# Optimization experiments

Measured on AMD Instinct MI355X. Metric: run time of the kernel, lower is better.

## Reference

```python
import jax, jax.numpy as jnp
import numpy as np

N_EXPERTS = 8
TOPK = 2
W_IMPORTANCE = 0.01
W_LOAD = 0.01
LAMBDA_Z = 0.001
W_PENALTY = 0.01
PENALTY_TEMP = 1.66


def setup_inputs() -> dict:
    key = jax.random.key(0)
    ks = jax.random.split(key, 8)
    B, S, D, H, E = 8, 4096, 512, 2048, N_EXPERTS
    T = B * S
    return {
        "x": jax.random.normal(ks[0], (B, S, D), dtype=jnp.float32),
        "gate_w": jax.random.normal(ks[1], (E, D), dtype=jnp.float32) * 0.02,
        "noise_w": jax.random.normal(ks[2], (E, D), dtype=jnp.float32) * 0.02,
        "bias": jnp.zeros((E,), dtype=jnp.float32),
        "c_fc_w": jax.random.normal(ks[3], (E, H, D), dtype=jnp.float32) * 0.02,
        "c_fc_b": jnp.zeros((E, H), dtype=jnp.float32),
        "c_proj_w": jax.random.normal(ks[4], (E, D, H), dtype=jnp.float32) * 0.02,
        "c_proj_b": jnp.zeros((E, D), dtype=jnp.float32),
        "noise": jax.random.normal(ks[5], (T, E), dtype=jnp.float32),
    }


def reference(x, gate_w, noise_w, bias, c_fc_w, c_fc_b, c_proj_w, c_proj_b, noise):
    E, K = N_EXPERTS, TOPK
    D = x.shape[-1]
    xs = x.reshape(-1, D)                      # [T, D]
    T = xs.shape[0]

    gate_logits = xs @ gate_w.T                # [T, E]

    # penalty (pre-noise logits)
    p = jax.nn.softmax(gate_logits / PENALTY_TEMP, axis=-1)
    penalty_a = jnp.mean(p * (1.0 - p))
    pm = p.mean(axis=0)
    penalty_b = 1.0 / E - jnp.mean(pm * (1.0 - pm))
    penalty = (penalty_a + penalty_b) * W_PENALTY

    # z-loss (pre-noise logits)
    lse = jax.scipy.special.logsumexp(gate_logits, axis=-1)
    z_loss = LAMBDA_Z * jnp.mean(lse ** 2)

    # noisy gating + bias
    noise_std = jax.nn.softplus(xs @ noise_w.T)
    gate_logits = gate_logits + noise * noise_std + bias

    weights_vals, selected = jax.lax.top_k(gate_logits, K)   # [T, K]
    weights = jax.nn.softmax(weights_vals.astype(jnp.float32), axis=1).astype(x.dtype)

    # importance loss: scatter-add weights per expert
    importance = jax.ops.segment_sum(weights.reshape(-1), selected.reshape(-1),
                                     num_segments=E)
    cv2 = jnp.var(importance) / jnp.mean(importance) ** 2
    importance_loss = W_IMPORTANCE * cv2

    # load loss: top-1 counts vs mean router probs (post-noise)
    router_probs = jax.nn.softmax(gate_logits.astype(jnp.float32), axis=-1).astype(x.dtype)
    top1 = selected[:, 0]
    fi = jax.ops.segment_sum(jnp.ones((T,), dtype=jnp.float32), top1,
                             num_segments=E) / T
    load_loss = W_LOAD * E * jnp.sum(fi * router_probs.mean(axis=0))

    aux = penalty + z_loss + importance_loss + load_loss

    # combine weights per (token, expert): [T, E]
    comb = jnp.zeros((T, E), dtype=x.dtype).at[jnp.arange(T)[:, None], selected].add(weights)

    results = jnp.zeros_like(xs)
    for e in range(E):  # fixed small expert count
        h = jax.nn.gelu(xs @ c_fc_w[e].T + c_fc_b[e], approximate=True)
        o = h @ c_proj_w[e].T + c_proj_b[e]
        results = results + comb[:, e:e + 1] * o

    return results.reshape(x.shape), aux
```

## Files before the change

kernel.cpp:

```cpp
#include <hip/hip_runtime.h>
#include <hip/hip_bf16.h>
#include <stdint.h>

#define TTOK 32768
#define DDIM 512
#define HDIM 2048
#define NEXP 8
#define GBLK 1024

typedef __attribute__((ext_vector_type(4))) float f32x4;
typedef __attribute__((ext_vector_type(8))) short bf16x8;

#define GLOAD16(gp, lp)                                                      \
  __builtin_amdgcn_global_load_lds(                                          \
      (const __attribute__((address_space(1))) unsigned int*)(gp),           \
      (__attribute__((address_space(3))) unsigned int*)(lp), 16, 0, 0)

__device__ __forceinline__ ushort f2bf(float f) {
  union { float f; uint32_t u; } cv; cv.f = f;
  uint32_t u = cv.u;
  u = u + 0x7fffu + ((u >> 16) & 1u);
  return (ushort)(u >> 16);
}

__device__ __forceinline__ float bf2f(ushort u) {
  union { uint32_t u; float f; } cv; cv.u = ((uint32_t)u) << 16;
  return cv.f;
}

__device__ __forceinline__ float gelu_fast(float v) {
  float y = 1.5957691216057308f * (v + 0.044715f * v * v * v);
  return v / (1.0f + __expf(-y));
}

__global__ __launch_bounds__(256) void cvtw_kernel(const float* __restrict__ src,
                                                   ushort* __restrict__ dst, int n4) {
  int i = blockIdx.x * blockDim.x + threadIdx.x;
  if (i >= n4) return;
  float4 v = reinterpret_cast<const float4*>(src)[i];
  ushort4 o;
  o.x = f2bf(v.x); o.y = f2bf(v.y); o.z = f2bf(v.z); o.w = f2bf(v.w);
  reinterpret_cast<ushort4*>(dst)[i] = o;
}

__global__ __launch_bounds__(256, 2) void gating_kernel(
    const float* __restrict__ x, const float* __restrict__ gw,
    const float* __restrict__ nw, const float* __restrict__ bias,
    const float* __restrict__ noise, ushort* __restrict__ xbf,
    int* __restrict__ cnt, int* __restrict__ idxl,
    int2* __restrict__ slots, float2* __restrict__ tokw,
    float* __restrict__ part) {
  const int tid = threadIdx.x;
  const int lane = tid & 63;
  const int wave = tid >> 6;

  float wg[NEXP][8], wn[NEXP][8];
#pragma unroll
  for (int e = 0; e < NEXP; ++e) {
    const float4* pg = reinterpret_cast<const float4*>(gw + e * DDIM + lane * 8);
    float4 g0 = pg[0], g1 = pg[1];
    wg[e][0] = g0.x; wg[e][1] = g0.y; wg[e][2] = g0.z; wg[e][3] = g0.w;
    wg[e][4] = g1.x; wg[e][5] = g1.y; wg[e][6] = g1.z; wg[e][7] = g1.w;
    const float4* pq = reinterpret_cast<const float4*>(nw + e * DDIM + lane * 8);
    float4 n0 = pq[0], n1 = pq[1];
    wn[e][0] = n0.x; wn[e][1] = n0.y; wn[e][2] = n0.z; wn[e][3] = n0.w;
    wn[e][4] = n1.x; wn[e][5] = n1.y; wn[e][6] = n1.z; wn[e][7] = n1.w;
  }
  float bia[NEXP];
#pragma unroll
  for (int e = 0; e < NEXP; ++e) bia[e] = bias[e];

  float pa_s = 0.f, z_s = 0.f;
  float pm_s[NEXP], imp_s[NEXP], rp_s[NEXP], c1_s[NEXP];
#pragma unroll
  for (int e = 0; e < NEXP; ++e) { pm_s[e] = 0.f; imp_s[e] = 0.f; rp_s[e] = 0.f; c1_s[e] = 0.f; }

  __shared__ int s_i1[32], s_i2[32];
  __shared__ float s_w1[32], s_w2[32];
  __shared__ int lcnt[NEXP], lpos1[32], lpos2[32], gbase[NEXP];

  const int t00 = blockIdx.x * 32 + wave * 8;
  for (int it = 0; it < 8; it += 2) {
    float xv[2][8], nz[2][8];
#pragma unroll
    for (int u = 0; u < 2; ++u) {
      const int t = t00 + it + u;
      const float4* np = reinterpret_cast<const float4*>(noise + (size_t)t * NEXP);
      float4 nz0 = np[0], nz1 = np[1];
      nz[u][0] = nz0.x; nz[u][1] = nz0.y; nz[u][2] = nz0.z; nz[u][3] = nz0.w;
      nz[u][4] = nz1.x; nz[u][5] = nz1.y; nz[u][6] = nz1.z; nz[u][7] = nz1.w;
      const float4* xp = reinterpret_cast<const float4*>(x + (size_t)t * DDIM + lane * 8);
      float4 x0 = xp[0], x1 = xp[1];
      xv[u][0] = x0.x; xv[u][1] = x0.y; xv[u][2] = x0.z; xv[u][3] = x0.w;
      xv[u][4] = x1.x; xv[u][5] = x1.y; xv[u][6] = x1.z; xv[u][7] = x1.w;
      ushort u8[8];
#pragma unroll
      for (int j = 0; j < 8; ++j) u8[j] = f2bf(xv[u][j]);
      uint4 pack;
      pack.x = (uint32_t)u8[0] | ((uint32_t)u8[1] << 16);
      pack.y = (uint32_t)u8[2] | ((uint32_t)u8[3] << 16);
      pack.z = (uint32_t)u8[4] | ((uint32_t)u8[5] << 16);
      pack.w = (uint32_t)u8[6] | ((uint32_t)u8[7] << 16);
      *reinterpret_cast<uint4*>(xbf + (size_t)t * DDIM + lane * 8) = pack;
    }

    float pg[2][NEXP], pn[2][NEXP];
#pragma unroll
    for (int u = 0; u < 2; ++u)
#pragma unroll
      for (int e = 0; e < NEXP; ++e) { pg[u][e] = 0.f; pn[u][e] = 0.f; }
#pragma unroll
    for (int e = 0; e < NEXP; ++e)
#pragma unroll
      for (int j = 0; j < 8; ++j) {
#pragma unroll
        for (int u = 0; u < 2; ++u) {
          pg[u][e] = fmaf(xv[u][j], wg[e][j], pg[u][e]);
          pn[u][e] = fmaf(xv[u][j], wn[e][j], pn[u][e]);
        }
      }
#pragma unroll
    for (int m = 1; m < 64; m <<= 1) {
#pragma unroll
      for (int u = 0; u < 2; ++u)
#pragma unroll
        for (int e = 0; e < NEXP; ++e) {
          pg[u][e] += __shfl_xor(pg[u][e], m);
          pn[u][e] += __shfl_xor(pn[u][e], m);
        }
    }

#pragma unroll
    for (int u = 0; u < 2; ++u) {
      const int t = t00 + it + u;
      float sv[NEXP];
#pragma unroll
      for (int e = 0; e < NEXP; ++e) sv[e] = pg[u][e] * (1.0f / 1.66f);
      float mx = sv[0];
#pragma unroll
      for (int e = 1; e < NEXP; ++e) mx = fmaxf(mx, sv[e]);
      float ssum = 0.f, pvals[NEXP];
#pragma unroll
      for (int e = 0; e < NEXP; ++e) { pvals[e] = __expf(sv[e] - mx); ssum += pvals[e]; }
      float sinv = 1.f / ssum;
#pragma unroll
      for (int e = 0; e < NEXP; ++e) {
        float pe = pvals[e] * sinv;
        pa_s += pe * (1.f - pe);
        pm_s[e] += pe;
      }
      float mg = pg[u][0];
#pragma unroll
      for (int e = 1; e < NEXP; ++e) mg = fmaxf(mg, pg[u][e]);
      float es2 = 0.f;
#pragma unroll
      for (int e = 0; e < NEXP; ++e) es2 += __expf(pg[u][e] - mg);
      float lse = mg + __logf(es2);
      z_s += lse * lse;
      float g2[NEXP];
#pragma unroll
      for (int e = 0; e < NEXP; ++e) {
        float s = pn[u][e];
        float sp = fmaxf(s, 0.f) + __logf(1.f + __expf(-fabsf(s)));
        g2[e] = pg[u][e] + nz[u][e] * sp + bia[e];
      }
      float v1 = g2[0]; int i1 = 0;
#pragma unroll
      for (int e = 1; e < NEXP; ++e) if (g2[e] > v1) { v1 = g2[e]; i1 = e; }
      float v2 = -3.4e38f; int i2 = 0;
#pragma unroll
      for (int e = 0; e < NEXP; ++e) if (e != i1 && g2[e] > v2) { v2 = g2[e]; i2 = e; }
      float dd = __expf(v2 - v1);
      float w1 = 1.f / (1.f + dd);
      float w2 = dd / (1.f + dd);
      float mr = g2[0];
#pragma unroll
      for (int e = 1; e < NEXP; ++e) mr = fmaxf(mr, g2[e]);
      float rs = 0.f, er[NEXP];
#pragma unroll
      for (int e = 0; e < NEXP; ++e) { er[e] = __expf(g2[e] - mr); rs += er[e]; }
      float rinv = 1.f / rs;
#pragma unroll
      for (int e = 0; e < NEXP; ++e) rp_s[e] += er[e] * rinv;
#pragma unroll
      for (int e = 0; e < NEXP; ++e) {
        imp_s[e] += (e == i1 ? w1 : 0.f) + (e == i2 ? w2 : 0.f);
        c1_s[e] += (e == i1) ? 1.f : 0.f;
      }
      if (lane == 0) {
        int k = wave * 8 + it + u;
        s_i1[k] = i1; s_i2[k] = i2; s_w1[k] = w1; s_w2[k] = w2;
      }
    }
  }

  __shared__ float red[4][34];
  if (lane == 0) {
    red[wave][0] = pa_s; red[wave][1] = z_s;
#pragma unroll
    for (int e = 0; e < NEXP; ++e) {
      red[wave][2 + e] = pm_s[e];
      red[wave][10 + e] = imp_s[e];
      red[wave][18 + e] = rp_s[e];
      red[wave][26 + e] = c1_s[e];
    }
  }
  if (tid < NEXP) lcnt[tid] = 0;
  __syncthreads();
  if (tid < 34) {
    float s = red[0][tid] + red[1][tid] + red[2][tid] + red[3][tid];
    part[(size_t)tid * GBLK + blockIdx.x] = s;
  }
  if (tid < 32) {
    lpos1[tid] = atomicAdd(&lcnt[s_i1[tid]], 1);
    lpos2[tid] = atomicAdd(&lcnt[s_i2[tid]], 1);
  }
  __syncthreads();
  if (tid < NEXP) gbase[tid] = atomicAdd(&cnt[tid], lcnt[tid]);
  __syncthreads();
  if (tid < 32) {
    int t = blockIdx.x * 32 + tid;
    int e1 = s_i1[tid], p1 = gbase[e1] + lpos1[tid];
    int e2 = s_i2[tid], p2 = gbase[e2] + lpos2[tid];
    idxl[e1 * TTOK + p1] = t;
    idxl[e2 * TTOK + p2] = t;
    slots[t] = make_int2((e1 << 16) | p1, (e2 << 16) | p2);
    tokw[t] = make_float2(s_w1[tid], s_w2[tid]);
  }
}

__global__ __launch_bounds__(256) void finalize_kernel(
    const float* __restrict__ part, const int* __restrict__ cnt,
    int* __restrict__ offs, int* __restrict__ idxl,
    float* __restrict__ aux_out) {
  __shared__ float sums[34];
  __shared__ float red[4][34];
  __shared__ int roundc[NEXP], base[NEXP];
  const int tid = threadIdx.x;
  const int lane = tid & 63, wave = tid >> 6;

  float loc[34];
#pragma unroll
  for (int s = 0; s < 34; ++s) loc[s] = 0.f;
  for (int b = tid; b < GBLK; b += 256) {
#pragma unroll
    for (int s = 0; s < 34; ++s) loc[s] += part[(size_t)s * GBLK + b];
  }
#pragma unroll
  for (int m = 1; m < 64; m <<= 1) {
#pragma unroll
    for (int s = 0; s < 34; ++s) loc[s] += __shfl_xor(loc[s], m);
  }
  if (lane == 0) {
#pragma unroll
    for (int s = 0; s < 34; ++s) red[wave][s] = loc[s];
  }
  if (tid == 0) {
    int acc = 0;
    for (int e = 0; e < NEXP; ++e) {
      int r = (cnt[e] + 127) & ~127;
      roundc[e] = r; base[e] = acc; acc += r;
    }
  }
  __syncthreads();
  if (tid < 34) sums[tid] = red[0][tid] + red[1][tid] + red[2][tid] + red[3][tid];
  __syncthreads();
  for (int i = tid; i < NEXP * 128; i += 256) {
    int e = i >> 7, k = i & 127;
    int pos = cnt[e] + k;
    if (pos < roundc[e]) idxl[e * TTOK + pos] = 0;
  }
  if (tid < NEXP) offs[tid] = base[tid];
  if (tid == 0) {
    const float Tf = (float)TTOK;
    float pa = sums[0] / (Tf * 8.f);
    float pbm = 0.f;
    for (int e = 0; e < NEXP; ++e) { float pm = sums[2 + e] / Tf; pbm += pm * (1.f - pm); }
    float pb = 1.f / 8.f - pbm / 8.f;
    float penalty = (pa + pb) * 0.01f;
    float z = 0.001f * sums[1] / Tf;
    float mean = 0.f;
    for (int e = 0; e < NEXP; ++e) mean += sums[10 + e];
    mean /= 8.f;
    float var = 0.f;
    for (int e = 0; e < NEXP; ++e) { float d = sums[10 + e] - mean; var += d * d; }
    var /= 8.f;
    float il = 0.01f * var / (mean * mean);
    float ld = 0.f;
    for (int e = 0; e < NEXP; ++e) ld += (sums[26 + e] / Tf) * (sums[18 + e] / Tf);
    ld *= 0.01f * 8.f;
    aux_out[0] = penalty + z + il + ld;
  }
}


__global__ __launch_bounds__(256, 2) void gemm1_kernel(
    const ushort* __restrict__ xbf, const ushort* __restrict__ wfc,
    const float* __restrict__ fcb, const int* __restrict__ idxl,
    const int* __restrict__ cnt, const int* __restrict__ offs,
    ushort* __restrict__ h, int hbase, int HC) {
  const int e = blockIdx.z;
  const int count = cnt[e];
  const int rounded = (count + 127) & ~127;
  const int mt = blockIdx.x;
  if (mt * 128 >= rounded) return;
  const int nt = blockIdx.y;
  const int tid = threadIdx.x;
  const int lane = tid & 63, wave = tid >> 6;
  const int wm = wave >> 1, wn = wave & 1;

  __shared__ ushort As[2][128][64];
  __shared__ ushort Bs[2][128][64];

  const int srow = tid >> 3;
  const int csw8 = (((tid & 7) ^ (srow & 7)) << 3);
  const int dst8 = ((tid & 7) << 3);

  int gA[4];
  const ushort* bbase = wfc + (size_t)e * (HDIM * DDIM) +
                        (size_t)(hbase + nt * 128) * DDIM;
#pragma unroll
  for (int r = 0; r < 4; ++r)
    gA[r] = idxl[e * TTOK + mt * 128 + srow + r * 32];

  f32x4 acc[4][4];
#pragma unroll
  for (int m = 0; m < 4; ++m)
#pragma unroll
    for (int n = 0; n < 4; ++n)
      acc[m][n] = (f32x4){0.f, 0.f, 0.f, 0.f};

#define G1_STAGE(buf, kt)                                                     \
  {                                                                           \
    const int koff = (kt) * 64;                                               \
    _Pragma("unroll") for (int r = 0; r < 4; ++r) {                           \
      GLOAD16(xbf + (size_t)gA[r] * DDIM + koff + csw8,                       \
              &As[buf][srow + r * 32][dst8]);                                 \
      GLOAD16(bbase + (size_t)(srow + r * 32) * DDIM + koff + csw8,           \
              &Bs[buf][srow + r * 32][dst8]);                                 \
    }                                                                         \
  }

  G1_STAGE(0, 0);
  asm volatile("s_waitcnt vmcnt(0)" ::: "memory");
  __syncthreads();

  const int NK = DDIM / 64;
  for (int kt = 0; kt < NK; ++kt) {
    const int cur = kt & 1;
    if (kt + 1 < NK) G1_STAGE(cur ^ 1, kt + 1);
#pragma unroll
    for (int ks = 0; ks < 2; ++ks) {
      const int ch = (((ks << 2) | (lane >> 4)) ^ (lane & 7)) << 3;
      bf16x8 af[4], bfr[4];
#pragma unroll
      for (int m = 0; m < 4; ++m)
        af[m] = *reinterpret_cast<const bf16x8*>(&As[cur][wm * 64 + m * 16 + (lane & 15)][ch]);
#pragma unroll
      for (int n = 0; n < 4; ++n)
        bfr[n] = *reinterpret_cast<const bf16x8*>(&Bs[cur][wn * 64 + n * 16 + (lane & 15)][ch]);
#pragma unroll
      for (int m = 0; m < 4; ++m)
#pragma unroll
        for (int n = 0; n < 4; ++n)
          acc[m][n] = __builtin_amdgcn_mfma_f32_16x16x32_bf16(af[m], bfr[n], acc[m][n], 0, 0, 0);
    }
    if (kt + 1 < NK) __syncthreads();
  }

  const int hb = offs[e];
#pragma unroll
  for (int n = 0; n < 4; ++n) {
    const int col = wn * 64 + n * 16 + (lane & 15);
    const int gcol = hbase + nt * 128 + col;
    const float bterm = fcb[e * HDIM + gcol];
#pragma unroll
    for (int m = 0; m < 4; ++m) {
#pragma unroll
      for (int j = 0; j < 4; ++j) {
        const int row = mt * 128 + wm * 64 + m * 16 + ((lane >> 4) << 2) + j;
        float v = acc[m][n][j] + bterm;
        h[(size_t)(hb + row) * HC + (nt * 128 + col)] = f2bf(gelu_fast(v));
      }
    }
  }
}

__global__ __launch_bounds__(256, 2) void gemm2_kernel(
    const ushort* __restrict__ h, const ushort* __restrict__ wpj,
    const float* __restrict__ pjb, const int* __restrict__ cnt,
    const int* __restrict__ offs, ushort* __restrict__ scratch,
    int hbase, int HC, int first_chunk) {
  const int e = blockIdx.z;
  const int count = cnt[e];
  const int rounded = (count + 127) & ~127;
  const int mt = blockIdx.x;
  if (mt * 128 >= rounded) return;
  const int nt = blockIdx.y;
  const int tid = threadIdx.x;
  const int lane = tid & 63, wave = tid >> 6;
  const int wm = wave >> 1, wn = wave & 1;

  __shared__ ushort As[2][128][64];
  __shared__ ushort Bs[2][128][64];

  const int srow = tid >> 3;
  const int csw8 = (((tid & 7) ^ (srow & 7)) << 3);
  const int dst8 = ((tid & 7) << 3);
  const int hb = offs[e];

  const ushort* abase = h + (size_t)(hb + mt * 128) * HC;
  const ushort* bbase = wpj + (size_t)e * (DDIM * HDIM) +
                        (size_t)(nt * 128) * HDIM + hbase;

  f32x4 acc[4][4];
#pragma unroll
  for (int m = 0; m < 4; ++m)
#pragma unroll
    for (int n = 0; n < 4; ++n)
      acc[m][n] = (f32x4){0.f, 0.f, 0.f, 0.f};

#define G2_STAGE(buf, kt)                                                     \
  {                                                                           \
    const int koff = (kt) * 64;                                               \
    _Pragma("unroll") for (int r = 0; r < 4; ++r) {                           \
      GLOAD16(abase + (size_t)(srow + r * 32) * HC + koff + csw8,             \
              &As[buf][srow + r * 32][dst8]);                                 \
      GLOAD16(bbase + (size_t)(srow + r * 32) * HDIM + koff + csw8,           \
              &Bs[buf][srow + r * 32][dst8]);                                 \
    }                                                                         \
  }

  G2_STAGE(0, 0);
  asm volatile("s_waitcnt vmcnt(0)" ::: "memory");
  __syncthreads();

  const int NK = HC / 64;
  for (int kt = 0; kt < NK; ++kt) {
    const int cur = kt & 1;
    if (kt + 1 < NK) G2_STAGE(cur ^ 1, kt + 1);
#pragma unroll
    for (int ks = 0; ks < 2; ++ks) {
      const int ch = (((ks << 2) | (lane >> 4)) ^ (lane & 7)) << 3;
      bf16x8 af[4], bfr[4];
#pragma unroll
      for (int m = 0; m < 4; ++m)
        af[m] = *reinterpret_cast<const bf16x8*>(&As[cur][wm * 64 + m * 16 + (lane & 15)][ch]);
#pragma unroll
      for (int n = 0; n < 4; ++n)
        bfr[n] = *reinterpret_cast<const bf16x8*>(&Bs[cur][wn * 64 + n * 16 + (lane & 15)][ch]);
#pragma unroll
      for (int m = 0; m < 4; ++m)
#pragma unroll
        for (int n = 0; n < 4; ++n)
          acc[m][n] = __builtin_amdgcn_mfma_f32_16x16x32_bf16(af[m], bfr[n], acc[m][n], 0, 0, 0);
    }
    if (kt + 1 < NK) __syncthreads();
  }

#pragma unroll
  for (int n = 0; n < 4; ++n) {
    const int col = nt * 128 + wn * 64 + n * 16 + (lane & 15);
    const float bterm = pjb[e * DDIM + col];
#pragma unroll
    for (int m = 0; m < 4; ++m) {
#pragma unroll
      for (int j = 0; j < 4; ++j) {
        const size_t row = (size_t)(hb + mt * 128 + wm * 64 + m * 16 + ((lane >> 4) << 2) + j);
        ushort* p = scratch + row * DDIM + col;
        float v = acc[m][n][j];
        if (first_chunk) v += bterm;
        else v += bf2f(*p);
        *p = f2bf(v);
      }
    }
  }
}

__global__ __launch_bounds__(256, 8) void combine_kernel(
    const ushort* __restrict__ scratch, const int* __restrict__ offs,
    const int2* __restrict__ slots, const float2* __restrict__ tokw,
    float* __restrict__ out) {
  const int lane = threadIdx.x & 63;
  const int wave = threadIdx.x >> 6;
  const int t = blockIdx.x * 4 + wave;
  int2 s = slots[t];
  float2 w = tokw[t];
  const int r1 = offs[s.x >> 16] + (s.x & 0xFFFF);
  const int r2 = offs[s.y >> 16] + (s.y & 0xFFFF);
  bf16x8 a = *reinterpret_cast<const bf16x8*>(scratch + (size_t)r1 * DDIM + lane * 8);
  bf16x8 b = *reinterpret_cast<const bf16x8*>(scratch + (size_t)r2 * DDIM + lane * 8);
  float r[8];
#pragma unroll
  for (int j = 0; j < 8; ++j)
    r[j] = w.x * bf2f((ushort)a[j]) + w.y * bf2f((ushort)b[j]);
  float4* op = reinterpret_cast<float4*>(out + (size_t)t * DDIM + lane * 8);
  op[0] = make_float4(r[0], r[1], r[2], r[3]);
  op[1] = make_float4(r[4], r[5], r[6], r[7]);
}

extern "C" void kernel_launch(void* const* d_in, const int* in_sizes, int n_in,
                              void* d_out, int out_size, void* d_ws, size_t ws_size,
                              hipStream_t stream) {
  const float* x    = (const float*)d_in[0];
  const float* gw   = (const float*)d_in[1];
  const float* nw   = (const float*)d_in[2];
  const float* bias = (const float*)d_in[3];
  const float* fcw  = (const float*)d_in[4];
  const float* fcb  = (const float*)d_in[5];
  const float* pjw  = (const float*)d_in[6];
  const float* pjb  = (const float*)d_in[7];
  const float* noise = (const float*)d_in[8];
  float* out = (float*)d_out;

  char* ws = (char*)d_ws;
  size_t o = 0;
  auto alloc = [&](size_t bytes) -> char* {
    char* p = ws + o;
    o += (bytes + 255) & ~(size_t)255;
    return p;
  };
  ushort* xbf   = (ushort*)alloc((size_t)TTOK * DDIM * 2);
  ushort* wfcb  = (ushort*)alloc((size_t)NEXP * HDIM * DDIM * 2);
  ushort* wpjb  = (ushort*)alloc((size_t)NEXP * DDIM * HDIM * 2);
  int*    idxl  = (int*)alloc((size_t)NEXP * TTOK * 4);
  int2*   slots = (int2*)alloc((size_t)TTOK * 8);
  float2* tokw  = (float2*)alloc((size_t)TTOK * 8);
  int*    cnt   = (int*)alloc(256);
  int*    offs  = (int*)alloc(256);
  float*  part  = (float*)alloc(34 * GBLK * 4);
  ushort* scr   = (ushort*)alloc((size_t)(2 * TTOK + 1024) * DDIM * 2);
  size_t fixed = o;

  int NCH = 16;
  const int chs[5] = {1, 2, 4, 8, 16};
  for (int ci = 0; ci < 5; ++ci) {
    size_t need = fixed + (size_t)(2 * TTOK + 1024) * (size_t)(HDIM / chs[ci]) * 2;
    if (need <= ws_size) { NCH = chs[ci]; break; }
  }
  const int HC = HDIM / NCH;
  ushort* h = (ushort*)alloc((size_t)(2 * TTOK + 1024) * HC * 2);

  hipMemsetAsync(cnt, 0, 32, stream);

  cvtw_kernel<<<8192, 256, 0, stream>>>(fcw, wfcb, NEXP * HDIM * DDIM / 4);
  cvtw_kernel<<<8192, 256, 0, stream>>>(pjw, wpjb, NEXP * DDIM * HDIM / 4);
  gating_kernel<<<GBLK, 256, 0, stream>>>(x, gw, nw, bias, noise, xbf, cnt, idxl, slots, tokw, part);
  finalize_kernel<<<1, 256, 0, stream>>>(part, cnt, offs, idxl, out + ((size_t)out_size - 1));

  for (int c = 0; c < NCH; ++c) {
    gemm1_kernel<<<dim3(256, HC / 128, NEXP), 256, 0, stream>>>(
        xbf, wfcb, fcb, idxl, cnt, offs, h, c * HC, HC);
    gemm2_kernel<<<dim3(256, 4, NEXP), 256, 0, stream>>>(
        h, wpjb, pjb, cnt, offs, scr, c * HC, HC, c == 0);
  }
  combine_kernel<<<TTOK / 4, 256, 0, stream>>>(scr, offs, slots, tokw, out);
}
```

Measured before the change: 794.4 us.

## Trade double buffering for higher occupancy in GEMMs; stage gating weights in LDS

Both grouped GEMM kernels drop their double-buffered LDS tiles for a single buffer, with load, wait and barrier every k-step. Launch bounds go from 2 to 4 blocks per CU so more waves can hide memory latency in place of software prefetch. The gating kernel now loads the gate and noise weights into shared memory instead of holding 128 floats per thread in registers, which cuts register pressure so it can run at higher occupancy. The risk is that losing the prefetch overlap exposes load latency, and the forced register cap could cause spills in the MFMA kernels.

```diff
diff --git a/kernel.cpp b/kernel.cpp
--- a/kernel.cpp
+++ b/kernel.cpp
@@ -43,7 +43,7 @@
   reinterpret_cast<ushort4*>(dst)[i] = o;
 }
 
-__global__ __launch_bounds__(256, 2) void gating_kernel(
+__global__ __launch_bounds__(256, 4) void gating_kernel(
     const float* __restrict__ x, const float* __restrict__ gw,
     const float* __restrict__ nw, const float* __restrict__ bias,
     const float* __restrict__ noise, ushort* __restrict__ xbf,
@@ -54,17 +54,12 @@
   const int lane = tid & 63;
   const int wave = tid >> 6;
 
-  float wg[NEXP][8], wn[NEXP][8];
-#pragma unroll
-  for (int e = 0; e < NEXP; ++e) {
-    const float4* pg = reinterpret_cast<const float4*>(gw + e * DDIM + lane * 8);
-    float4 g0 = pg[0], g1 = pg[1];
-    wg[e][0] = g0.x; wg[e][1] = g0.y; wg[e][2] = g0.z; wg[e][3] = g0.w;
-    wg[e][4] = g1.x; wg[e][5] = g1.y; wg[e][6] = g1.z; wg[e][7] = g1.w;
-    const float4* pq = reinterpret_cast<const float4*>(nw + e * DDIM + lane * 8);
-    float4 n0 = pq[0], n1 = pq[1];
-    wn[e][0] = n0.x; wn[e][1] = n0.y; wn[e][2] = n0.z; wn[e][3] = n0.w;
-    wn[e][4] = n1.x; wn[e][5] = n1.y; wn[e][6] = n1.z; wn[e][7] = n1.w;
+  __shared__ float wlds[2][NEXP][DDIM];
+  for (int i = tid; i < NEXP * DDIM / 4; i += 256) {
+    reinterpret_cast<float4*>(&wlds[0][0][0])[i] =
+        reinterpret_cast<const float4*>(gw)[i];
+    reinterpret_cast<float4*>(&wlds[1][0][0])[i] =
+        reinterpret_cast<const float4*>(nw)[i];
   }
   float bia[NEXP];
 #pragma unroll
@@ -78,6 +73,8 @@
   __shared__ int s_i1[32], s_i2[32];
   __shared__ float s_w1[32], s_w2[32];
   __shared__ int lcnt[NEXP], lpos1[32], lpos2[32], gbase[NEXP];
+  if (tid < NEXP) lcnt[tid] = 0;
+  __syncthreads();
 
   const int t00 = blockIdx.x * 32 + wave * 8;
   for (int it = 0; it < 8; it += 2) {
@@ -106,19 +103,24 @@
 
     float pg[2][NEXP], pn[2][NEXP];
 #pragma unroll
-    for (int u = 0; u < 2; ++u)
-#pragma unroll
-      for (int e = 0; e < NEXP; ++e) { pg[u][e] = 0.f; pn[u][e] = 0.f; }
-#pragma unroll
-    for (int e = 0; e < NEXP; ++e)
-#pragma unroll
-      for (int j = 0; j < 8; ++j) {
-#pragma unroll
-        for (int u = 0; u < 2; ++u) {
-          pg[u][e] = fmaf(xv[u][j], wg[e][j], pg[u][e]);
-          pn[u][e] = fmaf(xv[u][j], wn[e][j], pn[u][e]);
+    for (int e = 0; e < NEXP; ++e) {
+      const float4* wgp = reinterpret_cast<const float4*>(&wlds[0][e][lane * 8]);
+      float4 wg0 = wgp[0], wg1 = wgp[1];
+      const float4* wnp = reinterpret_cast<const float4*>(&wlds[1][e][lane * 8]);
+      float4 wn0 = wnp[0], wn1 = wnp[1];
+      float wge[8] = {wg0.x, wg0.y, wg0.z, wg0.w, wg1.x, wg1.y, wg1.z, wg1.w};
+      float wne[8] = {wn0.x, wn0.y, wn0.z, wn0.w, wn1.x, wn1.y, wn1.z, wn1.w};
+#pragma unroll
+      for (int u = 0; u < 2; ++u) {
+        float ag = 0.f, an = 0.f;
+#pragma unroll
+        for (int j = 0; j < 8; ++j) {
+          ag = fmaf(xv[u][j], wge[j], ag);
+          an = fmaf(xv[u][j], wne[j], an);
         }
-      }
+        pg[u][e] = ag; pn[u][e] = an;
+      }
+    }
 #pragma unroll
     for (int m = 1; m < 64; m <<= 1) {
 #pragma unroll
@@ -205,7 +207,6 @@
       red[wave][26 + e] = c1_s[e];
     }
   }
-  if (tid < NEXP) lcnt[tid] = 0;
   __syncthreads();
   if (tid < 34) {
     float s = red[0][tid] + red[1][tid] + red[2][tid] + red[3][tid];
@@ -294,7 +295,7 @@
 }
 
 
-__global__ __launch_bounds__(256, 2) void gemm1_kernel(
+__global__ __launch_bounds__(256, 4) void gemm1_kernel(
     const ushort* __restrict__ xbf, const ushort* __restrict__ wfc,
     const float* __restrict__ fcb, const int* __restrict__ idxl,
     const int* __restrict__ cnt, const int* __restrict__ offs,
@@ -309,8 +310,8 @@
   const int lane = tid & 63, wave = tid >> 6;
   const int wm = wave >> 1, wn = wave & 1;
 
-  __shared__ ushort As[2][128][64];
-  __shared__ ushort Bs[2][128][64];
+  __shared__ ushort As[128][64];
+  __shared__ ushort Bs[128][64];
 
   const int srow = tid >> 3;
   const int csw8 = (((tid & 7) ^ (srow & 7)) << 3);
@@ -330,42 +331,33 @@
     for (int n = 0; n < 4; ++n)
       acc[m][n] = (f32x4){0.f, 0.f, 0.f, 0.f};
 
-#define G1_STAGE(buf, kt)                                                     \
-  {                                                                           \
-    const int koff = (kt) * 64;                                               \
-    _Pragma("unroll") for (int r = 0; r < 4; ++r) {                           \
-      GLOAD16(xbf + (size_t)gA[r] * DDIM + koff + csw8,                       \
-              &As[buf][srow + r * 32][dst8]);                                 \
-      GLOAD16(bbase + (size_t)(srow + r * 32) * DDIM + koff + csw8,           \
-              &Bs[buf][srow + r * 32][dst8]);                                 \
-    }                                                                         \
-  }
-
-  G1_STAGE(0, 0);
-  asm volatile("s_waitcnt vmcnt(0)" ::: "memory");
-  __syncthreads();
-
   const int NK = DDIM / 64;
   for (int kt = 0; kt < NK; ++kt) {
-    const int cur = kt & 1;
-    if (kt + 1 < NK) G1_STAGE(cur ^ 1, kt + 1);
+    const int koff = kt * 64;
+#pragma unroll
+    for (int r = 0; r < 4; ++r) {
+      GLOAD16(xbf + (size_t)gA[r] * DDIM + koff + csw8, &As[srow + r * 32][dst8]);
+      GLOAD16(bbase + (size_t)(srow + r * 32) * DDIM + koff + csw8, &Bs[srow + r * 32][dst8]);
+    }
+    asm volatile("s_waitcnt vmcnt(0)" ::: "memory");
+    __syncthreads();
 #pragma unroll
     for (int ks = 0; ks < 2; ++ks) {
       const int ch = (((ks << 2) | (lane >> 4)) ^ (lane & 7)) << 3;
       bf16x8 af[4], bfr[4];
 #pragma unroll
       for (int m = 0; m < 4; ++m)
-        af[m] = *reinterpret_cast<const bf16x8*>(&As[cur][wm * 64 + m * 16 + (lane & 15)][ch]);
+        af[m] = *reinterpret_cast<const bf16x8*>(&As[wm * 64 + m * 16 + (lane & 15)][ch]);
 #pragma unroll
       for (int n = 0; n < 4; ++n)
-        bfr[n] = *reinterpret_cast<const bf16x8*>(&Bs[cur][wn * 64 + n * 16 + (lane & 15)][ch]);
+        bfr[n] = *reinterpret_cast<const bf16x8*>(&Bs[wn * 64 + n * 16 + (lane & 15)][ch]);
 #pragma unroll
       for (int m = 0; m < 4; ++m)
 #pragma unroll
         for (int n = 0; n < 4; ++n)
           acc[m][n] = __builtin_amdgcn_mfma_f32_16x16x32_bf16(af[m], bfr[n], acc[m][n], 0, 0, 0);
     }
-    if (kt + 1 < NK) __syncthreads();
+    __syncthreads();
   }
 
   const int hb = offs[e];
@@ -386,7 +378,7 @@
   }
 }
 
-__global__ __launch_bounds__(256, 2) void gemm2_kernel(
+__global__ __launch_bounds__(256, 4) void gemm2_kernel(
     const ushort* __restrict__ h, const ushort* __restrict__ wpj,
     const float* __restrict__ pjb, const int* __restrict__ cnt,
     const int* __restrict__ offs, ushort* __restrict__ scratch,
@@ -401,8 +393,8 @@
   const int lane = tid & 63, wave = tid >> 6;
   const int wm = wave >> 1, wn = wave & 1;
 
-  __shared__ ushort As[2][128][64];
-  __shared__ ushort Bs[2][128][64];
+  __shared__ ushort As[128][64];
+  __shared__ ushort Bs[128][64];
 
   const int srow = tid >> 3;
   const int csw8 = (((tid & 7) ^ (srow & 7)) << 3);
@@ -420,42 +412,33 @@
     for (int n = 0; n < 4; ++n)
       acc[m][n] = (f32x4){0.f, 0.f, 0.f, 0.f};
 
-#define G2_STAGE(buf, kt)                                                     \
-  {                                                                           \
-    const int koff = (kt) * 64;                                               \
-    _Pragma("unroll") for (int r = 0; r < 4; ++r) {                           \
-      GLOAD16(abase + (size_t)(srow + r * 32) * HC + koff + csw8,             \
-              &As[buf][srow + r * 32][dst8]);                                 \
-      GLOAD16(bbase + (size_t)(srow + r * 32) * HDIM + koff + csw8,           \
-              &Bs[buf][srow + r * 32][dst8]);                                 \
-    }                                                                         \
-  }
-
-  G2_STAGE(0, 0);
-  asm volatile("s_waitcnt vmcnt(0)" ::: "memory");
-  __syncthreads();
-
   const int NK = HC / 64;
   for (int kt = 0; kt < NK; ++kt) {
-    const int cur = kt & 1;
-    if (kt + 1 < NK) G2_STAGE(cur ^ 1, kt + 1);
+    const int koff = kt * 64;
+#pragma unroll
+    for (int r = 0; r < 4; ++r) {
+      GLOAD16(abase + (size_t)(srow + r * 32) * HC + koff + csw8, &As[srow + r * 32][dst8]);
+      GLOAD16(bbase + (size_t)(srow + r * 32) * HDIM + koff + csw8, &Bs[srow + r * 32][dst8]);
+    }
+    asm volatile("s_waitcnt vmcnt(0)" ::: "memory");
+    __syncthreads();
 #pragma unroll
     for (int ks = 0; ks < 2; ++ks) {
       const int ch = (((ks << 2) | (lane >> 4)) ^ (lane & 7)) << 3;
       bf16x8 af[4], bfr[4];
 #pragma unroll
       for (int m = 0; m < 4; ++m)
-        af[m] = *reinterpret_cast<const bf16x8*>(&As[cur][wm * 64 + m * 16 + (lane & 15)][ch]);
+        af[m] = *reinterpret_cast<const bf16x8*>(&As[wm * 64 + m * 16 + (lane & 15)][ch]);
 #pragma unroll
       for (int n = 0; n < 4; ++n)
-        bfr[n] = *reinterpret_cast<const bf16x8*>(&Bs[cur][wn * 64 + n * 16 + (lane & 15)][ch]);
+        bfr[n] = *reinterpret_cast<const bf16x8*>(&Bs[wn * 64 + n * 16 + (lane & 15)][ch]);
 #pragma unroll
       for (int m = 0; m < 4; ++m)
 #pragma unroll
         for (int n = 0; n < 4; ++n)
           acc[m][n] = __builtin_amdgcn_mfma_f32_16x16x32_bf16(af[m], bfr[n], acc[m][n], 0, 0, 0);
     }
-    if (kt + 1 < NK) __syncthreads();
+    __syncthreads();
   }
 
 #pragma unroll
```

Measured after the change: 897.9 us. +13.0%, slower.
